# Kernel optimization log

Hardware: AMD Instinct MI355X
Metric: run time of the kernel (lower is better)

The kernel has to match this reference:

```python
import jax, jax.numpy as jnp
import numpy as np

B, S, I, H, C = 256, 128, 512, 1024, 10
VOCAB = S  # nn.Embedding(seq_length, input_dim)


def _lstm_dir(embeds_tbi, W, b):
    """Run an LSTM over time. embeds_tbi: [S,B,I]; W: [4H, I+H] stacked (g,i,f,o); b: [4H]."""
    h0 = jnp.zeros((B, H), jnp.float32)
    c0 = jnp.zeros((B, H), jnp.float32)

    def step(carry, x_t):
        c, h = carry
        xh = jnp.concatenate([x_t, h], axis=1)          # [B, I+H]
        z = xh @ W.T + b                                 # [B, 4H]
        g, i, f, o = jnp.split(z, 4, axis=1)
        g = jnp.tanh(g)
        i = jax.nn.sigmoid(i)
        f = jax.nn.sigmoid(f)
        o = jax.nn.sigmoid(o)
        new_c = g * i + c * f
        new_h = jnp.tanh(new_c) * o
        return (new_c, new_h), None

    (c_T, h_T), _ = jax.lax.scan(step, (c0, h0), embeds_tbi)
    return h_T


def setup_inputs() -> dict:
    key = jax.random.key(0)
    ks = jax.random.split(key, 8)
    x = jax.random.randint(ks[0], (B, S), 0, VOCAB)
    embed = jax.random.normal(ks[1], (VOCAB, I), jnp.float32) * 0.5
    scale = 1.0 / np.sqrt(I + H)
    fwd_W = jax.random.normal(ks[2], (4 * H, I + H), jnp.float32) * scale  # stacked g,i,f,o
    fwd_b = jax.random.normal(ks[3], (4 * H,), jnp.float32) * 0.02
    bwd_W = jax.random.normal(ks[4], (4 * H, I + H), jnp.float32) * scale
    bwd_b = jax.random.normal(ks[5], (4 * H,), jnp.float32) * 0.02
    p_w = jax.random.normal(ks[6], (C, 2 * H), jnp.float32) * (1.0 / np.sqrt(2 * H))
    p_b = jax.random.normal(ks[7], (C,), jnp.float32) * 0.02
    return {"x": x, "embed": embed, "fwd_W": fwd_W, "fwd_b": fwd_b,
            "bwd_W": bwd_W, "bwd_b": bwd_b, "p_w": p_w, "p_b": p_b}


def reference(x, embed, fwd_W, fwd_b, bwd_W, bwd_b, p_w, p_b):
    embeds = embed[x]                       # [B,S,I]
    emb_t = jnp.transpose(embeds, (1, 0, 2))  # [S,B,I]
    h_fwd = _lstm_dir(emb_t, fwd_W, fwd_b)
    h_bwd = _lstm_dir(emb_t[::-1], bwd_W, bwd_b)
    h_comb = jnp.concatenate([h_fwd, h_bwd], axis=1)  # [B,2H]
    return jax.nn.log_softmax(h_comb @ p_w.T + p_b, axis=1)
```

## Files before the change

### kernel.cpp

```cpp
#include <hip/hip_runtime.h>
#include <hip/hip_bf16.h>
#include <math.h>

#define B 256
#define S 128
#define I_DIM 512
#define H 1024
#define C 10
#define WROW 1536

#define LDS_H 131072

typedef float f32x4 __attribute__((ext_vector_type(4), may_alias));
typedef __bf16 bf16x8 __attribute__((ext_vector_type(8), may_alias));
typedef unsigned int u32x4 __attribute__((ext_vector_type(4), may_alias));
typedef unsigned long long u64;
typedef unsigned long long __attribute__((may_alias)) u64a;

__device__ __forceinline__ unsigned short f2bf(float f) {
    union { float f; unsigned u; } a; a.f = f;
    return (unsigned short)((a.u + 0x7fffu + ((a.u >> 16) & 1u)) >> 16);
}
__device__ __forceinline__ float bf2f(unsigned short b) {
    union { unsigned u; float f; } a; a.u = ((unsigned)b) << 16;
    return a.f;
}
__device__ __forceinline__ float sigf(float v) { return 1.0f / (1.0f + __expf(-v)); }
__device__ __forceinline__ float tanh_fast(float v) { return 1.0f - 2.0f / (1.0f + __expf(2.0f * v)); }

__global__ void prep_build(const float* __restrict__ fwd_W,
                           const float* __restrict__ bwd_W,
                           const float* __restrict__ embed,
                           __hip_bfloat16* __restrict__ wF,
                           __hip_bfloat16* __restrict__ wxF,
                           unsigned short* __restrict__ ehl) {
    int gid = blockIdx.x * 256 + threadIdx.x;
    if (gid < 1048576) {
        int lane = gid & 63, kk = (gid >> 6) & 31, nsub = (gid >> 11) & 255, d = gid >> 19;
        int n_gl = nsub * 16 + (lane & 15);
        int j = n_gl >> 2, g = n_gl & 3;
        int k = kk * 32 + (lane >> 4) * 8;
        const float* W = d ? bwd_W : fwd_W;
        const float* src = W + (size_t)(g * 1024 + j) * WROW + I_DIM + k;
        ushort4 lo = make_ushort4(f2bf(src[0]), f2bf(src[1]), f2bf(src[2]), f2bf(src[3]));
        ushort4 hi = make_ushort4(f2bf(src[4]), f2bf(src[5]), f2bf(src[6]), f2bf(src[7]));
        ushort4* dst = (ushort4*)(wF + (size_t)gid * 8);
        dst[0] = lo; dst[1] = hi;
    } else if (gid < 1048576 + 524288) {
        int g2 = gid - 1048576;
        int lane = g2 & 63, kk = (g2 >> 6) & 15, nsub = (g2 >> 10) & 255, d = g2 >> 18;
        int n_gl = nsub * 16 + (lane & 15);
        int j = n_gl >> 2, g = n_gl & 3;
        int k = kk * 32 + (lane >> 4) * 8;
        const float* W = d ? bwd_W : fwd_W;
        const float* src = W + (size_t)(g * 1024 + j) * WROW + k;
        ushort4 lo = make_ushort4(f2bf(src[0]), f2bf(src[1]), f2bf(src[2]), f2bf(src[3]));
        ushort4 hi = make_ushort4(f2bf(src[4]), f2bf(src[5]), f2bf(src[6]), f2bf(src[7]));
        ushort4* dst = (ushort4*)(wxF + (size_t)g2 * 8);
        dst[0] = lo; dst[1] = hi;
    } else {
        int idx = gid - (1048576 + 524288);
        float e = embed[idx];
        unsigned short hb = f2bf(e);
        unsigned short lb = f2bf(e - bf2f(hb));
        ehl[idx] = hb;
        ehl[65536 + idx] = lb;
    }
}

__global__ __launch_bounds__(256) void projp_mfma(
        const __hip_bfloat16* __restrict__ wxF,
        const unsigned short* __restrict__ ehl,
        const float* __restrict__ fwd_b,
        const float* __restrict__ bwd_b,
        float* __restrict__ projP) {
    extern __shared__ char sm[];
    const int bid = blockIdx.x;
    const int d = bid >> 7, jt = (bid >> 2) & 31, vb = bid & 3;
    const int tid = threadIdx.x, w = tid >> 6, lane = tid & 63;
    const int l15 = lane & 15, l4 = lane >> 4;
    const int v0 = vb * 32;

    for (int i = 0; i < 16; i++) {
        int chunk = i * 256 + tid;
        int row = chunk >> 6, c16 = chunk & 63;
        int p = row >> 5, vs = v0 + (row & 31);
        u32x4 vd = *(const u32x4*)(ehl + ((size_t)p * 128 + vs) * 512 + c16 * 8);
        *(u32x4*)(sm + row * 1024 + ((c16 * 16) ^ ((row & 7) << 4))) = vd;
    }
    __syncthreads();

    const __hip_bfloat16* ap0 = wxF + ((size_t)((d * 256 + jt * 8 + w * 2 + 0) * 16)) * 512;
    const __hip_bfloat16* ap1 = wxF + ((size_t)((d * 256 + jt * 8 + w * 2 + 1) * 16)) * 512;
    int hrow[2], hswz[2], lrow[2], lswz[2];
#pragma unroll
    for (int vt = 0; vt < 2; vt++) {
        int hr = vt * 16 + l15, lr = hr + 32;
        hrow[vt] = hr * 1024; hswz[vt] = (hr & 7) << 4;
        lrow[vt] = lr * 1024; lswz[vt] = (lr & 7) << 4;
    }
    f32x4 acc[2][2] = {};
#pragma unroll
    for (int kk = 0; kk < 16; kk++) {
        bf16x8 A0 = *(const bf16x8*)(ap0 + kk * 512 + lane * 8);
        bf16x8 A1 = *(const bf16x8*)(ap1 + kk * 512 + lane * 8);
        int ko = kk * 64 + l4 * 16;
        bf16x8 Bh0 = *(const bf16x8*)(sm + hrow[0] + (ko ^ hswz[0]));
        bf16x8 Bh1 = *(const bf16x8*)(sm + hrow[1] + (ko ^ hswz[1]));
        bf16x8 Bl0 = *(const bf16x8*)(sm + lrow[0] + (ko ^ lswz[0]));
        bf16x8 Bl1 = *(const bf16x8*)(sm + lrow[1] + (ko ^ lswz[1]));
        acc[0][0] = __builtin_amdgcn_mfma_f32_16x16x32_bf16(A0, Bh0, acc[0][0], 0, 0, 0);
        acc[0][0] = __builtin_amdgcn_mfma_f32_16x16x32_bf16(A0, Bl0, acc[0][0], 0, 0, 0);
        acc[0][1] = __builtin_amdgcn_mfma_f32_16x16x32_bf16(A0, Bh1, acc[0][1], 0, 0, 0);
        acc[0][1] = __builtin_amdgcn_mfma_f32_16x16x32_bf16(A0, Bl1, acc[0][1], 0, 0, 0);
        acc[1][0] = __builtin_amdgcn_mfma_f32_16x16x32_bf16(A1, Bh0, acc[1][0], 0, 0, 0);
        acc[1][0] = __builtin_amdgcn_mfma_f32_16x16x32_bf16(A1, Bl0, acc[1][0], 0, 0, 0);
        acc[1][1] = __builtin_amdgcn_mfma_f32_16x16x32_bf16(A1, Bh1, acc[1][1], 0, 0, 0);
        acc[1][1] = __builtin_amdgcn_mfma_f32_16x16x32_bf16(A1, Bl1, acc[1][1], 0, 0, 0);
    }
    const float* bp = d ? bwd_b : fwd_b;
#pragma unroll
    for (int nt = 0; nt < 2; nt++) {
        int j = jt * 32 + w * 8 + nt * 4 + l4;
        f32x4 bv = { bp[j], bp[1024 + j], bp[2048 + j], bp[3072 + j] };
#pragma unroll
        for (int vt = 0; vt < 2; vt++) {
            int v = v0 + vt * 16 + l15;
            *(f32x4*)(projP + ((size_t)(d * 1024 + j) * 128 + v) * 4) = acc[nt][vt] + bv;
        }
    }
}

__global__ __launch_bounds__(512, 1) void step_kernel(
        const int* __restrict__ x,
        const __hip_bfloat16* __restrict__ wF,
        const float* __restrict__ projP,
        __hip_bfloat16* __restrict__ hbuf,
        float* __restrict__ cws,
        int t) {
    extern __shared__ char smem[];
    const int bid = blockIdx.x;
    const int d = bid >> 7, bt = (bid >> 5) & 3, jt = bid & 31;
    const int tid = threadIdx.x, wid = tid >> 6, lane = tid & 63;
    const int l15 = lane & 15, l4 = lane >> 4;
    const int b0 = bt * 64;
    const size_t dBH = (size_t)d * B * H;

    if (t > 0) {
        const char* hrb = (const char*)(hbuf + (size_t)(t & 1) * 2 * B * H + dBH + (size_t)b0 * H);
#if __has_builtin(__builtin_amdgcn_global_load_lds)
#pragma unroll
        for (int i = 0; i < 16; i++) {
            int r = i * 8 + wid;
            int row = r >> 1, half = r & 1;
            int m = half * 64 + lane;
            const void* src = hrb + row * 2048 + ((m ^ (row & 7)) << 4);
            __builtin_amdgcn_global_load_lds(
                (const __attribute__((address_space(1))) void*)src,
                (__attribute__((address_space(3))) void*)(smem + row * 2048 + half * 1024),
                16, 0, 0);
        }
#else
#pragma unroll
        for (int i = 0; i < 16; i++) {
            int flat = i * 512 + tid;
            int row = flat >> 7, c16 = flat & 127;
            u32x4 v = *(const u32x4*)(hrb + (size_t)row * 2048 + c16 * 16);
            *(u32x4*)(smem + row * 2048 + ((c16 * 16) ^ ((row & 7) << 4))) = v;
        }
#endif
        __syncthreads();
    }

    f32x4 acc[4] = {};
    if (t > 0) {
        const __hip_bfloat16* wp = wF + (size_t)(d * 256 + jt * 8 + wid) * 16384;
        int brow[4], bswz[4];
#pragma unroll
        for (int bs = 0; bs < 4; bs++) {
            int row = bs * 16 + l15;
            brow[bs] = row * 2048;
            bswz[bs] = (row & 7) << 4;
        }
        bf16x8 Acur = *(const bf16x8*)(wp + lane * 8);
        bf16x8 Bcur[4];
#pragma unroll
        for (int bs = 0; bs < 4; bs++)
            Bcur[bs] = *(const bf16x8*)(smem + brow[bs] + ((l4 * 16) ^ bswz[bs]));
#pragma unroll
        for (int kk = 0; kk < 32; kk++) {
            bf16x8 A = Acur;
            bf16x8 B0 = Bcur[0], B1 = Bcur[1], B2 = Bcur[2], B3 = Bcur[3];
            if (kk < 31) {
                Acur = *(const bf16x8*)(wp + (kk + 1) * 512 + lane * 8);
                int koff = (kk + 1) * 64 + l4 * 16;
#pragma unroll
                for (int bs = 0; bs < 4; bs++)
                    Bcur[bs] = *(const bf16x8*)(smem + brow[bs] + (koff ^ bswz[bs]));
            }
            acc[0] = __builtin_amdgcn_mfma_f32_16x16x32_bf16(A, B0, acc[0], 0, 0, 0);
            acc[1] = __builtin_amdgcn_mfma_f32_16x16x32_bf16(A, B1, acc[1], 0, 0, 0);
            acc[2] = __builtin_amdgcn_mfma_f32_16x16x32_bf16(A, B2, acc[2], 0, 0, 0);
            acc[3] = __builtin_amdgcn_mfma_f32_16x16x32_bf16(A, B3, acc[3], 0, 0, 0);
        }
    }

    const int tt = d ? (S - 1 - t) : t;
    const int j = jt * 32 + wid * 4 + l4;
    const f32x4* pp = (const f32x4*)projP + ((size_t)d * 1024 + j) * 128;
    f32x4 pj[4];
#pragma unroll
    for (int bs = 0; bs < 4; bs++) {
        int v = x[(b0 + bs * 16 + l15) * S + tt];
        pj[bs] = pp[v];
    }

    float* cp = cws + ((size_t)bid * 512 + tid) * 4;
    f32x4 cv = {0.f, 0.f, 0.f, 0.f};
    if (t > 0) cv = *(const f32x4*)cp;

    float hnv[4];
#pragma unroll
    for (int bs = 0; bs < 4; bs++) {
        float zg = acc[bs][0] + pj[bs][0];
        float zi = acc[bs][1] + pj[bs][1];
        float zf = acc[bs][2] + pj[bs][2];
        float zo = acc[bs][3] + pj[bs][3];
        float gg = tanh_fast(zg);
        float ii = sigf(zi);
        float ff = sigf(zf);
        float oo = sigf(zo);
        float cn = gg * ii + cv[bs] * ff;
        cv[bs] = cn;
        hnv[bs] = tanh_fast(cn) * oo;
    }
    *(f32x4*)cp = cv;

    unsigned plo = (unsigned)f2bf(hnv[0]) | ((unsigned)f2bf(hnv[1]) << 16);
    unsigned phi = (unsigned)f2bf(hnv[2]) | ((unsigned)f2bf(hnv[3]) << 16);
    unsigned short o4[4];
#pragma unroll
    for (int p = 0; p < 4; p++) {
        int src = p * 16 + l15;
        unsigned vlo = __shfl(plo, src);
        unsigned vhi = __shfl(phi, src);
        unsigned sel = (l4 < 2) ? vlo : vhi;
        o4[p] = (l4 & 1) ? (unsigned short)(sel >> 16) : (unsigned short)(sel & 0xffffu);
    }
    u64 hv = (u64)o4[0] | ((u64)o4[1] << 16) | ((u64)o4[2] << 32) | ((u64)o4[3] << 48);
    __hip_bfloat16* hw = hbuf + (size_t)((t + 1) & 1) * 2 * B * H + dBH
                         + (size_t)(b0 + lane) * H + jt * 32 + wid * 4;
    *(u64a*)hw = hv;
}

__global__ void head_kernel(const __hip_bfloat16* __restrict__ hbuf,
                            const float* __restrict__ p_w,
                            const float* __restrict__ p_b,
                            float* __restrict__ out) {
    int b = blockIdx.x;
    int lane = threadIdx.x;
    float part[C];
#pragma unroll
    for (int cc = 0; cc < C; cc++) part[cc] = 0.0f;
    for (int jj = lane; jj < 2 * H; jj += 64) {
        float hv = (jj < H)
            ? __bfloat162float(hbuf[(size_t)b * H + jj])
            : __bfloat162float(hbuf[(size_t)B * H + (size_t)b * H + jj - H]);
#pragma unroll
        for (int cc = 0; cc < C; cc++) part[cc] += hv * p_w[cc * 2 * H + jj];
    }
#pragma unroll
    for (int cc = 0; cc < C; cc++) {
        float v = part[cc];
        for (int off = 32; off; off >>= 1) v += __shfl_down(v, off);
        part[cc] = v;
    }
    if (lane == 0) {
        float lg[C];
        float m = -1e30f;
        for (int cc = 0; cc < C; cc++) {
            lg[cc] = part[cc] + p_b[cc];
            m = fmaxf(m, lg[cc]);
        }
        float s = 0.0f;
        for (int cc = 0; cc < C; cc++) s += expf(lg[cc] - m);
        float lse = logf(s) + m;
        for (int cc = 0; cc < C; cc++) out[b * C + cc] = lg[cc] - lse;
    }
}

extern "C" void kernel_launch(void* const* d_in, const int* in_sizes, int n_in,
                              void* d_out, int out_size, void* d_ws, size_t ws_size,
                              hipStream_t stream) {
    const int*   x     = (const int*)d_in[0];
    const float* embed = (const float*)d_in[1];
    const float* fwd_W = (const float*)d_in[2];
    const float* fwd_b = (const float*)d_in[3];
    const float* bwd_W = (const float*)d_in[4];
    const float* bwd_b = (const float*)d_in[5];
    const float* p_w   = (const float*)d_in[6];
    const float* p_b   = (const float*)d_in[7];
    float* outp = (float*)d_out;

    char* ws = (char*)d_ws;
    __hip_bfloat16* wF  = (__hip_bfloat16*)ws;  ws += (size_t)2 * 256 * 16384 * 2;
    __hip_bfloat16* wxF = (__hip_bfloat16*)ws;
    float* cws = (float*)ws;                    ws += (size_t)2 * 256 * 8192 * 2;
    unsigned short* ehl = (unsigned short*)ws;  ws += (size_t)2 * 128 * 512 * 2;
    float* projP = (float*)ws;                  ws += (size_t)2 * 1024 * 128 * 4 * 4;
    __hip_bfloat16* hbuf = (__hip_bfloat16*)ws; ws += (size_t)2 * 2 * B * H * 2;

    hipLaunchKernelGGL(prep_build, dim3(6400), dim3(256), 0, stream,
                       fwd_W, bwd_W, embed, wF, wxF, ehl);

    hipFuncSetAttribute((const void*)projp_mfma,
                        hipFuncAttributeMaxDynamicSharedMemorySize, 65536);
    hipLaunchKernelGGL(projp_mfma, dim3(256), dim3(256), 65536, stream,
                       wxF, ehl, fwd_b, bwd_b, projP);

    hipFuncSetAttribute((const void*)step_kernel,
                        hipFuncAttributeMaxDynamicSharedMemorySize, LDS_H);
    for (int t = 0; t < S; t++)
        hipLaunchKernelGGL(step_kernel, dim3(256), dim3(512), LDS_H, stream,
                           x, wF, projP, hbuf, cws, t);

    hipLaunchKernelGGL(head_kernel, dim3(B), dim3(64), 0, stream,
                       hbuf, p_w, p_b, outp);
}
```

Before: 1.414 ms.

## Retile step kernel warps into 2x2 MFMA fragments and prefetch weights before h load

Each warp now computes a 2 (weight rows) by 2 (batch slices) tile of MFMA outputs instead of a 1x4 tile. This halves the LDS reads of h per warp in exchange for twice as many global weight loads. The first weight fragments are also issued before the hidden-state copy into LDS and its barrier, to overlap global latency. The gate indexing, projection lookup, shuffle packing and h writeback are remapped to match the new fragment layout.

```diff
diff --git a/kernel.cpp b/kernel.cpp
--- a/kernel.cpp
+++ b/kernel.cpp
@@ -142,9 +142,19 @@
     const int bid = blockIdx.x;
     const int d = bid >> 7, bt = (bid >> 5) & 3, jt = bid & 31;
     const int tid = threadIdx.x, wid = tid >> 6, lane = tid & 63;
+    const int ngrp = wid >> 1, bgrp = wid & 1;
     const int l15 = lane & 15, l4 = lane >> 4;
     const int b0 = bt * 64;
     const size_t dBH = (size_t)d * B * H;
+
+    const __hip_bfloat16* wp0 = wF + (size_t)(d * 256 + jt * 8 + ngrp * 2) * 16384;
+    const __hip_bfloat16* wp1 = wp0 + 16384;
+
+    bf16x8 A0c, A1c;
+    if (t > 0) {
+        A0c = *(const bf16x8*)(wp0 + lane * 8);
+        A1c = *(const bf16x8*)(wp1 + lane * 8);
+    }
 
     if (t > 0) {
         const char* hrb = (const char*)(hbuf + (size_t)(t & 1) * 2 * B * H + dBH + (size_t)b0 * H);
@@ -172,84 +182,88 @@
         __syncthreads();
     }
 
-    f32x4 acc[4] = {};
+    f32x4 acc[2][2] = {};
     if (t > 0) {
-        const __hip_bfloat16* wp = wF + (size_t)(d * 256 + jt * 8 + wid) * 16384;
-        int brow[4], bswz[4];
-#pragma unroll
-        for (int bs = 0; bs < 4; bs++) {
-            int row = bs * 16 + l15;
+        int brow[2], bswz[2];
+#pragma unroll
+        for (int bs = 0; bs < 2; bs++) {
+            int row = bgrp * 32 + bs * 16 + l15;
             brow[bs] = row * 2048;
             bswz[bs] = (row & 7) << 4;
         }
-        bf16x8 Acur = *(const bf16x8*)(wp + lane * 8);
-        bf16x8 Bcur[4];
-#pragma unroll
-        for (int bs = 0; bs < 4; bs++)
-            Bcur[bs] = *(const bf16x8*)(smem + brow[bs] + ((l4 * 16) ^ bswz[bs]));
+        bf16x8 B0c = *(const bf16x8*)(smem + brow[0] + ((l4 * 16) ^ bswz[0]));
+        bf16x8 B1c = *(const bf16x8*)(smem + brow[1] + ((l4 * 16) ^ bswz[1]));
 #pragma unroll
         for (int kk = 0; kk < 32; kk++) {
-            bf16x8 A = Acur;
-            bf16x8 B0 = Bcur[0], B1 = Bcur[1], B2 = Bcur[2], B3 = Bcur[3];
+            bf16x8 A0 = A0c, A1 = A1c, Bb0 = B0c, Bb1 = B1c;
             if (kk < 31) {
-                Acur = *(const bf16x8*)(wp + (kk + 1) * 512 + lane * 8);
+                A0c = *(const bf16x8*)(wp0 + (kk + 1) * 512 + lane * 8);
+                A1c = *(const bf16x8*)(wp1 + (kk + 1) * 512 + lane * 8);
                 int koff = (kk + 1) * 64 + l4 * 16;
-#pragma unroll
-                for (int bs = 0; bs < 4; bs++)
-                    Bcur[bs] = *(const bf16x8*)(smem + brow[bs] + (koff ^ bswz[bs]));
+                B0c = *(const bf16x8*)(smem + brow[0] + (koff ^ bswz[0]));
+                B1c = *(const bf16x8*)(smem + brow[1] + (koff ^ bswz[1]));
             }
-            acc[0] = __builtin_amdgcn_mfma_f32_16x16x32_bf16(A, B0, acc[0], 0, 0, 0);
-            acc[1] = __builtin_amdgcn_mfma_f32_16x16x32_bf16(A, B1, acc[1], 0, 0, 0);
-            acc[2] = __builtin_amdgcn_mfma_f32_16x16x32_bf16(A, B2, acc[2], 0, 0, 0);
-            acc[3] = __builtin_amdgcn_mfma_f32_16x16x32_bf16(A, B3, acc[3], 0, 0, 0);
+            acc[0][0] = __builtin_amdgcn_mfma_f32_16x16x32_bf16(A0, Bb0, acc[0][0], 0, 0, 0);
+            acc[0][1] = __builtin_amdgcn_mfma_f32_16x16x32_bf16(A0, Bb1, acc[0][1], 0, 0, 0);
+            acc[1][0] = __builtin_amdgcn_mfma_f32_16x16x32_bf16(A1, Bb0, acc[1][0], 0, 0, 0);
+            acc[1][1] = __builtin_amdgcn_mfma_f32_16x16x32_bf16(A1, Bb1, acc[1][1], 0, 0, 0);
         }
     }
 
     const int tt = d ? (S - 1 - t) : t;
-    const int j = jt * 32 + wid * 4 + l4;
-    const f32x4* pp = (const f32x4*)projP + ((size_t)d * 1024 + j) * 128;
-    f32x4 pj[4];
-#pragma unroll
-    for (int bs = 0; bs < 4; bs++) {
-        int v = x[(b0 + bs * 16 + l15) * S + tt];
-        pj[bs] = pp[v];
+    int vv[2];
+#pragma unroll
+    for (int bs = 0; bs < 2; bs++)
+        vv[bs] = x[(b0 + bgrp * 32 + bs * 16 + l15) * S + tt];
+    f32x4 pj[2][2];
+#pragma unroll
+    for (int frag = 0; frag < 2; frag++) {
+        int j = jt * 32 + ngrp * 8 + frag * 4 + l4;
+        const f32x4* pp = (const f32x4*)projP + ((size_t)d * 1024 + j) * 128;
+#pragma unroll
+        for (int bs = 0; bs < 2; bs++) pj[frag][bs] = pp[vv[bs]];
     }
 
     float* cp = cws + ((size_t)bid * 512 + tid) * 4;
     f32x4 cv = {0.f, 0.f, 0.f, 0.f};
     if (t > 0) cv = *(const f32x4*)cp;
 
-    float hnv[4];
-#pragma unroll
-    for (int bs = 0; bs < 4; bs++) {
-        float zg = acc[bs][0] + pj[bs][0];
-        float zi = acc[bs][1] + pj[bs][1];
-        float zf = acc[bs][2] + pj[bs][2];
-        float zo = acc[bs][3] + pj[bs][3];
-        float gg = tanh_fast(zg);
-        float ii = sigf(zi);
-        float ff = sigf(zf);
-        float oo = sigf(zo);
-        float cn = gg * ii + cv[bs] * ff;
-        cv[bs] = cn;
-        hnv[bs] = tanh_fast(cn) * oo;
-    }
+    float hnv[2][2];
+#pragma unroll
+    for (int frag = 0; frag < 2; frag++)
+#pragma unroll
+        for (int bs = 0; bs < 2; bs++) {
+            float zg = acc[frag][bs][0] + pj[frag][bs][0];
+            float zi = acc[frag][bs][1] + pj[frag][bs][1];
+            float zf = acc[frag][bs][2] + pj[frag][bs][2];
+            float zo = acc[frag][bs][3] + pj[frag][bs][3];
+            float gg = tanh_fast(zg);
+            float ii = sigf(zi);
+            float ff = sigf(zf);
+            float oo = sigf(zo);
+            int ci = frag * 2 + bs;
+            float cn = gg * ii + cv[ci] * ff;
+            cv[ci] = cn;
+            hnv[frag][bs] = tanh_fast(cn) * oo;
+        }
     *(f32x4*)cp = cv;
 
-    unsigned plo = (unsigned)f2bf(hnv[0]) | ((unsigned)f2bf(hnv[1]) << 16);
-    unsigned phi = (unsigned)f2bf(hnv[2]) | ((unsigned)f2bf(hnv[3]) << 16);
+    unsigned wA = (unsigned)f2bf(hnv[0][0]) | ((unsigned)f2bf(hnv[0][1]) << 16);
+    unsigned wB = (unsigned)f2bf(hnv[1][0]) | ((unsigned)f2bf(hnv[1][1]) << 16);
     unsigned short o4[4];
 #pragma unroll
     for (int p = 0; p < 4; p++) {
         int src = p * 16 + l15;
-        unsigned vlo = __shfl(plo, src);
-        unsigned vhi = __shfl(phi, src);
-        unsigned sel = (l4 < 2) ? vlo : vhi;
-        o4[p] = (l4 & 1) ? (unsigned short)(sel >> 16) : (unsigned short)(sel & 0xffffu);
+        unsigned va = __shfl(wA, src);
+        unsigned vb = __shfl(wB, src);
+        unsigned sel = (lane >= 32) ? vb : va;
+        o4[p] = ((lane >> 4) & 1) ? (unsigned short)(sel >> 16)
+                                  : (unsigned short)(sel & 0xffffu);
     }
     u64 hv = (u64)o4[0] | ((u64)o4[1] << 16) | ((u64)o4[2] << 32) | ((u64)o4[3] << 48);
     __hip_bfloat16* hw = hbuf + (size_t)((t + 1) & 1) * 2 * B * H + dBH
-                         + (size_t)(b0 + lane) * H + jt * 32 + wid * 4;
+                         + (size_t)(b0 + bgrp * 32 + (lane & 31)) * H
+                         + jt * 32 + ngrp * 8 + (lane >> 5) * 4;
     *(u64a*)hw = hv;
 }
 
```

Result: slower. 1.659 ms (+17.3%).
